# Kernel optimization log

Measured on AMD Instinct MI355X. Metric: run time of the kernel, lower is better.

Reference implementation:

```python
import jax, jax.numpy as jnp
import numpy as np

B, L, D = 8, 4096, 256
H, C = 2, 128
DEG = 16  # incoming ring neighbors per node (excluding self loop)


def _build_edge_index():
    # Block-diagonal graph replicated per batch element, like _get_buffer.
    i = np.arange(L)
    offs = np.arange(1, DEG + 1)
    src_g = ((i[:, None] + offs[None, :]) % L).reshape(-1)   # [L*DEG]
    dst_g = np.repeat(i, DEG)                                 # [L*DEG]
    base = (np.arange(B) * L)[:, None]
    src = (src_g[None, :] + base).reshape(-1)
    dst = (dst_g[None, :] + base).reshape(-1)
    # PyG GATConv: remove_self_loops + add_self_loops -> exactly one self loop/node
    self_idx = np.arange(B * L)
    src = np.concatenate([src, self_idx])
    dst = np.concatenate([dst, self_idx])
    return jnp.asarray(np.stack([src, dst]), dtype=jnp.int32)  # [2, E]


def setup_inputs() -> dict:
    key = jax.random.key(0)
    k0, k1, k2, k3 = jax.random.split(key, 4)
    glorot = 1.0 / np.sqrt(D)
    return {
        "x": jax.random.normal(k0, (B, L, D), jnp.float32),
        "edge_index": _build_edge_index(),
        "W": jax.random.normal(k1, (D, H * C), jnp.float32) * glorot,
        "att_src": jax.random.normal(k2, (H, C), jnp.float32) * (1.0 / np.sqrt(C)),
        "att_dst": jax.random.normal(k3, (H, C), jnp.float32) * (1.0 / np.sqrt(C)),
        "bias": jnp.zeros((H * C,), jnp.float32),
    }


def reference(x, edge_index, W, att_src, att_dst, bias):
    b, l, d = x.shape
    n = b * l
    h_, c_ = att_src.shape
    xf = x.reshape(n, d)                                   # flatten batch of graphs
    res = xf
    h = (xf @ W).reshape(n, h_, c_)                        # [N,H,C] projected features
    a_src = jnp.einsum('nhc,hc->nh', h, att_src)           # per-node src logits
    a_dst = jnp.einsum('nhc,hc->nh', h, att_dst)
    s, t = edge_index[0], edge_index[1]
    alpha = jax.nn.leaky_relu(a_src[s] + a_dst[t], 0.2)    # [E,H]
    # softmax over incoming edges of each destination node
    amax = jax.ops.segment_max(alpha, t, num_segments=n)
    ex = jnp.exp(alpha - amax[t])
    denom = jax.ops.segment_sum(ex, t, num_segments=n)
    attn = ex / jnp.where(denom[t] > 0, denom[t], 1.0)     # [E,H]
    msg = h[s] * attn[:, :, None]                          # [E,H,C]
    out = jax.ops.segment_sum(msg, t, num_segments=n).reshape(n, h_ * c_) + bias
    out = jax.nn.relu(out) + res                           # relu + residual
    return out.reshape(b, l, h_ * c_)
```

## Files before the change

kernel.cpp:

```cpp
#include <hip/hip_runtime.h>

#define LL 4096
#define DD 256
#define TM 64
#define HALO 16
#define ROWS (TM + HALO)
#define NTH 512
#define APAD 40
#define HTS 104
#define WBS 104
#define ABUF_BYTES (ROWS * APAD * 2)

typedef float f32x4 __attribute__((ext_vector_type(4)));
typedef __bf16 bf16x8 __attribute__((ext_vector_type(8)));
typedef unsigned short us8 __attribute__((ext_vector_type(8)));
typedef unsigned short us4 __attribute__((ext_vector_type(4)));

__device__ __forceinline__ unsigned short f2bf(float f) {
    union { float f; unsigned u; } v; v.f = f;
    unsigned r = v.u + 0x7fffu + ((v.u >> 16) & 1u);
    return (unsigned short)(r >> 16);
}

__global__ void prep_w(const float* __restrict__ W, unsigned short* __restrict__ Wt) {
    int t = blockIdx.x * blockDim.x + threadIdx.x;
    int l = t & 63;
    int kk = (t >> 6) & 7;
    int ct = t >> 9;
    int col = (ct << 4) + (l & 15);
    int kbase = kk * 32 + ((l >> 4) << 3);
    us8 v;
    for (int j = 0; j < 8; ++j) v[j] = f2bf(W[(kbase + j) * 256 + col]);
    *reinterpret_cast<us8*>(Wt + t * 8) = v;
}

__global__ __launch_bounds__(NTH, 4) void gat_fused(
    const float* __restrict__ x, const unsigned short* __restrict__ Wt,
    const float* __restrict__ att_src, const float* __restrict__ att_dst,
    const float* __restrict__ bias, float* __restrict__ out)
{
    __shared__ unsigned short h_t[256][HTS];
    __shared__ float alog[ROWS][2][2];
    __shared__ __align__(16) unsigned char smem_u[2 * 64 * WBS * 2];
    unsigned short (*abuf0)[APAD] = reinterpret_cast<unsigned short(*)[APAD]>(smem_u);
    unsigned short (*abuf1)[APAD] = reinterpret_cast<unsigned short(*)[APAD]>(smem_u + ABUF_BYTES);
    unsigned short (*wband)[WBS]  = reinterpret_cast<unsigned short(*)[WBS]>(smem_u);

    const int tid  = threadIdx.x;
    const int lane = tid & 63;
    const int wv   = tid >> 6;
    const int lo   = lane & 15;
    const int hi   = lane >> 4;
    const int blk  = blockIdx.x;
    const int batch = blk >> 6;
    const int i0    = (blk & 63) * TM;
    const long xbase = (long)batch * (LL * DD);
    const int ct0 = wv * 2;
    const int hd  = wv >> 2;

    {
        int chan = tid >> 1, half = tid & 1;
        us8 z = {0, 0, 0, 0, 0, 0, 0, 0};
        *reinterpret_cast<us8*>(&h_t[chan][80 + half * 8]) = z;
        if (tid < 320) ((float*)alog)[tid] = 0.f;
    }

    f32x4 acc[5][2];
    for (int a = 0; a < 5; ++a)
        for (int b = 0; b < 2; ++b)
            acc[a][b] = (f32x4){0.f, 0.f, 0.f, 0.f};

    const int s0r = tid >> 3, s0k = (tid & 7) << 2;
    const int s1r = (tid + 512) >> 3, s1k = ((tid + 512) & 7) << 2;
    const float* xrow0 = x + xbase + (long)((i0 + s0r) & (LL - 1)) * DD + s0k;
    const float* xrow1 = x + xbase + (long)((i0 + s1r) & (LL - 1)) * DD + s1k;
    const unsigned short* wtb0 = Wt + (size_t)(ct0 * 8 * 64 + lane) * 8;
    const unsigned short* wtb1 = Wt + (size_t)((ct0 + 1) * 8 * 64 + lane) * 8;

    float4 cur0, cur1, nxt0, nxt1;
    us8 braw0, braw1, nbraw0, nbraw1;

    cur0 = *reinterpret_cast<const float4*>(xrow0);
    if (tid < 128) cur1 = *reinterpret_cast<const float4*>(xrow1);
    braw0 = *reinterpret_cast<const us8*>(wtb0);
    braw1 = *reinterpret_cast<const us8*>(wtb1);
    {
        us4 p;
        p[0] = f2bf(cur0.x); p[1] = f2bf(cur0.y); p[2] = f2bf(cur0.z); p[3] = f2bf(cur0.w);
        *reinterpret_cast<us4*>(&abuf0[s0r][s0k]) = p;
        if (tid < 128) {
            us4 q;
            q[0] = f2bf(cur1.x); q[1] = f2bf(cur1.y); q[2] = f2bf(cur1.z); q[3] = f2bf(cur1.w);
            *reinterpret_cast<us4*>(&abuf0[s1r][s1k]) = q;
        }
    }

#pragma unroll
    for (int kk = 0; kk < 8; ++kk) {
        unsigned short (*buf)[APAD]  = (kk & 1) ? abuf1 : abuf0;
        unsigned short (*nbuf)[APAD] = (kk & 1) ? abuf0 : abuf1;
        if (kk < 7) {
            nxt0 = *reinterpret_cast<const float4*>(xrow0 + (kk + 1) * 32);
            if (tid < 128) nxt1 = *reinterpret_cast<const float4*>(xrow1 + (kk + 1) * 32);
            nbraw0 = *reinterpret_cast<const us8*>(wtb0 + (size_t)(kk + 1) * 64 * 8);
            nbraw1 = *reinterpret_cast<const us8*>(wtb1 + (size_t)(kk + 1) * 64 * 8);
        }
        __syncthreads();

        bf16x8 bfrag0 = __builtin_bit_cast(bf16x8, braw0);
        bf16x8 bfrag1 = __builtin_bit_cast(bf16x8, braw1);
        for (int rt = 0; rt < 5; ++rt) {
            us8 araw = *reinterpret_cast<const us8*>(&buf[rt * 16 + lo][hi * 8]);
            bf16x8 afrag = __builtin_bit_cast(bf16x8, araw);
            acc[rt][0] = __builtin_amdgcn_mfma_f32_16x16x32_bf16(bfrag0, afrag, acc[rt][0], 0, 0, 0);
            acc[rt][1] = __builtin_amdgcn_mfma_f32_16x16x32_bf16(bfrag1, afrag, acc[rt][1], 0, 0, 0);
        }

        if (kk < 7) {
            us4 p;
            p[0] = f2bf(nxt0.x); p[1] = f2bf(nxt0.y); p[2] = f2bf(nxt0.z); p[3] = f2bf(nxt0.w);
            *reinterpret_cast<us4*>(&nbuf[s0r][s0k]) = p;
            if (tid < 128) {
                us4 q;
                q[0] = f2bf(nxt1.x); q[1] = f2bf(nxt1.y); q[2] = f2bf(nxt1.z); q[3] = f2bf(nxt1.w);
                *reinterpret_cast<us4*>(&nbuf[s1r][s1k]) = q;
            }
            braw0 = nbraw0;
            braw1 = nbraw1;
        }
    }

    {
        const float4 as0 = *reinterpret_cast<const float4*>(att_src + ct0 * 16 + hi * 4);
        const float4 as1 = *reinterpret_cast<const float4*>(att_src + (ct0 + 1) * 16 + hi * 4);
        const float4 ad0 = *reinterpret_cast<const float4*>(att_dst + ct0 * 16 + hi * 4);
        const float4 ad1 = *reinterpret_cast<const float4*>(att_dst + (ct0 + 1) * 16 + hi * 4);

        float ps[5], pd[5];
        for (int rt = 0; rt < 5; ++rt) {
            f32x4 a0 = acc[rt][0], a1 = acc[rt][1];
            ps[rt] = a0[0] * as0.x + a0[1] * as0.y + a0[2] * as0.z + a0[3] * as0.w
                   + a1[0] * as1.x + a1[1] * as1.y + a1[2] * as1.z + a1[3] * as1.w;
            pd[rt] = a0[0] * ad0.x + a0[1] * ad0.y + a0[2] * ad0.z + a0[3] * ad0.w
                   + a1[0] * ad1.x + a1[1] * ad1.y + a1[2] * ad1.z + a1[3] * ad1.w;
            int xrow = rt * 16 + lo;
            for (int j = 0; j < 4; ++j)
                h_t[ct0 * 16 + hi * 4 + j][xrow] = f2bf(a0[j]);
            for (int j = 0; j < 4; ++j)
                h_t[(ct0 + 1) * 16 + hi * 4 + j][xrow] = f2bf(a1[j]);
        }
        for (int rt = 0; rt < 5; ++rt) {
            ps[rt] += __shfl_xor(ps[rt], 16);
            ps[rt] += __shfl_xor(ps[rt], 32);
            pd[rt] += __shfl_xor(pd[rt], 16);
            pd[rt] += __shfl_xor(pd[rt], 32);
        }
        if (hi == 0) {
            for (int rt = 0; rt < 5; ++rt) {
                atomicAdd(&alog[rt * 16 + lo][hd][0], ps[rt]);
                atomicAdd(&alog[rt * 16 + lo][hd][1], pd[rt]);
            }
        }
    }

    float4 res[4][2];
    for (int rt = 0; rt < 4; ++rt)
        for (int c = 0; c < 2; ++c)
            res[rt][c] = *reinterpret_cast<const float4*>(
                x + xbase + (long)(i0 + rt * 16 + lo) * DD + (ct0 + c) * 16 + hi * 4);

    __syncthreads();

    if (tid < 128) {
        int r = tid >> 1, h2 = tid & 1;
        unsigned short* wrow = &wband[h2 * 64 + r][0];
        us8 z = {0, 0, 0, 0, 0, 0, 0, 0};
        for (int q = 0; q < 13; ++q) *reinterpret_cast<us8*>(wrow + q * 8) = z;
        float ad = alog[r][h2][1];
        float al[17];
        float mx = -1e30f;
        for (int k = 0; k < 17; ++k) {
            float s = (k < 16) ? alog[r + 1 + k][h2][0] : alog[r][h2][0];
            float v = s + ad;
            v = (v > 0.f) ? v : 0.2f * v;
            al[k] = v;
            mx = fmaxf(mx, v);
        }
        float sum = 0.f;
        for (int k = 0; k < 17; ++k) { al[k] = __expf(al[k] - mx); sum += al[k]; }
        float inv = 1.f / sum;
        wrow[r] = f2bf(al[16] * inv);
        for (int k = 0; k < 16; ++k) wrow[r + 1 + k] = f2bf(al[k] * inv);
    }
    __syncthreads();

    {
        f32x4 acc2[4][2];
        for (int a = 0; a < 4; ++a)
            for (int b = 0; b < 2; ++b)
                acc2[a][b] = (f32x4){0.f, 0.f, 0.f, 0.f};

        for (int kq = 0; kq < 3; ++kq) {
            bf16x8 bfr[4];
            for (int rt = 0; rt < 4; ++rt) {
                us8 raw = *reinterpret_cast<const us8*>(
                    &wband[hd * 64 + rt * 16 + lo][kq * 32 + hi * 8]);
                bfr[rt] = __builtin_bit_cast(bf16x8, raw);
            }
            for (int c = 0; c < 2; ++c) {
                us8 araw = *reinterpret_cast<const us8*>(
                    &h_t[(ct0 + c) * 16 + lo][kq * 32 + hi * 8]);
                bf16x8 afr = __builtin_bit_cast(bf16x8, araw);
                for (int rt = 0; rt < 4; ++rt)
                    acc2[rt][c] = __builtin_amdgcn_mfma_f32_16x16x32_bf16(afr, bfr[rt], acc2[rt][c], 0, 0, 0);
            }
        }

        const float4 b40 = *reinterpret_cast<const float4*>(bias + ct0 * 16 + hi * 4);
        const float4 b41 = *reinterpret_cast<const float4*>(bias + (ct0 + 1) * 16 + hi * 4);
        for (int rt = 0; rt < 4; ++rt)
            for (int c = 0; c < 2; ++c) {
                const float4 b4 = c ? b41 : b40;
                f32x4 s = acc2[rt][c];
                long g = xbase + (long)(i0 + rt * 16 + lo) * DD + (ct0 + c) * 16 + hi * 4;
                float4 o;
                o.x = fmaxf(s[0] + b4.x, 0.f) + res[rt][c].x;
                o.y = fmaxf(s[1] + b4.y, 0.f) + res[rt][c].y;
                o.z = fmaxf(s[2] + b4.z, 0.f) + res[rt][c].z;
                o.w = fmaxf(s[3] + b4.w, 0.f) + res[rt][c].w;
                *reinterpret_cast<float4*>(out + g) = o;
            }
    }
}

extern "C" void kernel_launch(void* const* d_in, const int* in_sizes, int n_in,
                              void* d_out, int out_size, void* d_ws, size_t ws_size,
                              hipStream_t stream) {
    const float* x       = (const float*)d_in[0];
    const float* W       = (const float*)d_in[2];
    const float* att_src = (const float*)d_in[3];
    const float* att_dst = (const float*)d_in[4];
    const float* bias    = (const float*)d_in[5];
    float* out           = (float*)d_out;
    unsigned short* Wt   = (unsigned short*)d_ws;

    hipLaunchKernelGGL(prep_w, dim3(32), dim3(256), 0, stream, W, Wt);
    hipLaunchKernelGGL(gat_fused, dim3(512), dim3(NTH), 0, stream,
                       x, Wt, att_src, att_dst, bias, out);
}
```

Before: 32.52 us.

## Issue all x and W global loads upfront and use packed bf16 convert

All eight K-step tiles of x rows and W fragments are now loaded into registers before the MFMA loop, instead of prefetching one step ahead. This gives all global loads more time to be in flight while the MFMAs run. The manual bf16 rounding is also replaced with the hardware v_cvt_pk_bf16_f32 instruction, which packs two values per instruction. The cost is much higher VGPR pressure (about 64 floats plus 64 bf16 words per thread), which at 512 threads with launch bounds of 4 could cause spills or lower occupancy.

```diff
diff --git a/kernel.cpp b/kernel.cpp
--- a/kernel.cpp
+++ b/kernel.cpp
@@ -15,11 +15,18 @@
 typedef __bf16 bf16x8 __attribute__((ext_vector_type(8)));
 typedef unsigned short us8 __attribute__((ext_vector_type(8)));
 typedef unsigned short us4 __attribute__((ext_vector_type(4)));
+typedef unsigned int u32x2 __attribute__((ext_vector_type(2)));
 
 __device__ __forceinline__ unsigned short f2bf(float f) {
     union { float f; unsigned u; } v; v.f = f;
     unsigned r = v.u + 0x7fffu + ((v.u >> 16) & 1u);
     return (unsigned short)(r >> 16);
+}
+
+__device__ __forceinline__ unsigned cvtpk_bf16(float a, float b) {
+    unsigned r;
+    asm("v_cvt_pk_bf16_f32 %0, %1, %2" : "=v"(r) : "v"(a), "v"(b));
+    return r;
 }
 
 __global__ void prep_w(const float* __restrict__ W, unsigned short* __restrict__ Wt) {
@@ -77,21 +84,32 @@
     const unsigned short* wtb0 = Wt + (size_t)(ct0 * 8 * 64 + lane) * 8;
     const unsigned short* wtb1 = Wt + (size_t)((ct0 + 1) * 8 * 64 + lane) * 8;
 
-    float4 cur0, cur1, nxt0, nxt1;
-    us8 braw0, braw1, nbraw0, nbraw1;
-
-    cur0 = *reinterpret_cast<const float4*>(xrow0);
-    if (tid < 128) cur1 = *reinterpret_cast<const float4*>(xrow1);
-    braw0 = *reinterpret_cast<const us8*>(wtb0);
-    braw1 = *reinterpret_cast<const us8*>(wtb1);
-    {
-        us4 p;
-        p[0] = f2bf(cur0.x); p[1] = f2bf(cur0.y); p[2] = f2bf(cur0.z); p[3] = f2bf(cur0.w);
-        *reinterpret_cast<us4*>(&abuf0[s0r][s0k]) = p;
+    us8 br0[8], br1[8];
+#pragma unroll
+    for (int kk = 0; kk < 8; ++kk) {
+        br0[kk] = *reinterpret_cast<const us8*>(wtb0 + (size_t)kk * 64 * 8);
+        br1[kk] = *reinterpret_cast<const us8*>(wtb1 + (size_t)kk * 64 * 8);
+    }
+    float4 v0[8], v1[8];
+#pragma unroll
+    for (int kk = 0; kk < 8; ++kk)
+        v0[kk] = *reinterpret_cast<const float4*>(xrow0 + kk * 32);
+    if (tid < 128) {
+#pragma unroll
+        for (int kk = 0; kk < 8; ++kk)
+            v1[kk] = *reinterpret_cast<const float4*>(xrow1 + kk * 32);
+    }
+
+    {
+        u32x2 p;
+        p[0] = cvtpk_bf16(v0[0].x, v0[0].y);
+        p[1] = cvtpk_bf16(v0[0].z, v0[0].w);
+        *reinterpret_cast<u32x2*>(&abuf0[s0r][s0k]) = p;
         if (tid < 128) {
-            us4 q;
-            q[0] = f2bf(cur1.x); q[1] = f2bf(cur1.y); q[2] = f2bf(cur1.z); q[3] = f2bf(cur1.w);
-            *reinterpret_cast<us4*>(&abuf0[s1r][s1k]) = q;
+            u32x2 q;
+            q[0] = cvtpk_bf16(v1[0].x, v1[0].y);
+            q[1] = cvtpk_bf16(v1[0].z, v1[0].w);
+            *reinterpret_cast<u32x2*>(&abuf0[s1r][s1k]) = q;
         }
     }
 
@@ -99,16 +117,10 @@
     for (int kk = 0; kk < 8; ++kk) {
         unsigned short (*buf)[APAD]  = (kk & 1) ? abuf1 : abuf0;
         unsigned short (*nbuf)[APAD] = (kk & 1) ? abuf0 : abuf1;
-        if (kk < 7) {
-            nxt0 = *reinterpret_cast<const float4*>(xrow0 + (kk + 1) * 32);
-            if (tid < 128) nxt1 = *reinterpret_cast<const float4*>(xrow1 + (kk + 1) * 32);
-            nbraw0 = *reinterpret_cast<const us8*>(wtb0 + (size_t)(kk + 1) * 64 * 8);
-            nbraw1 = *reinterpret_cast<const us8*>(wtb1 + (size_t)(kk + 1) * 64 * 8);
-        }
         __syncthreads();
 
-        bf16x8 bfrag0 = __builtin_bit_cast(bf16x8, braw0);
-        bf16x8 bfrag1 = __builtin_bit_cast(bf16x8, braw1);
+        bf16x8 bfrag0 = __builtin_bit_cast(bf16x8, br0[kk]);
+        bf16x8 bfrag1 = __builtin_bit_cast(bf16x8, br1[kk]);
         for (int rt = 0; rt < 5; ++rt) {
             us8 araw = *reinterpret_cast<const us8*>(&buf[rt * 16 + lo][hi * 8]);
             bf16x8 afrag = __builtin_bit_cast(bf16x8, araw);
@@ -117,16 +129,16 @@
         }
 
         if (kk < 7) {
-            us4 p;
-            p[0] = f2bf(nxt0.x); p[1] = f2bf(nxt0.y); p[2] = f2bf(nxt0.z); p[3] = f2bf(nxt0.w);
-            *reinterpret_cast<us4*>(&nbuf[s0r][s0k]) = p;
+            u32x2 p;
+            p[0] = cvtpk_bf16(v0[kk + 1].x, v0[kk + 1].y);
+            p[1] = cvtpk_bf16(v0[kk + 1].z, v0[kk + 1].w);
+            *reinterpret_cast<u32x2*>(&nbuf[s0r][s0k]) = p;
             if (tid < 128) {
-                us4 q;
-                q[0] = f2bf(nxt1.x); q[1] = f2bf(nxt1.y); q[2] = f2bf(nxt1.z); q[3] = f2bf(nxt1.w);
-                *reinterpret_cast<us4*>(&nbuf[s1r][s1k]) = q;
-            }
-            braw0 = nbraw0;
-            braw1 = nbraw1;
+                u32x2 q;
+                q[0] = cvtpk_bf16(v1[kk + 1].x, v1[kk + 1].y);
+                q[1] = cvtpk_bf16(v1[kk + 1].z, v1[kk + 1].w);
+                *reinterpret_cast<u32x2*>(&nbuf[s1r][s1k]) = q;
+            }
         }
     }
 
```

New measurement: 46.76 us. +43.8%, slower.
